# Kernel optimization log

Hardware: AMD Instinct MI355X
Metric: run time of the kernel (lower is better)

## Reference

```python
import jax, jax.numpy as jnp
import numpy as np

B, S, H, E, V = 16, 512, 1024, 256, 50257


def setup_inputs() -> dict:
    key = jax.random.key(0)
    ks = jax.random.split(key, 16)
    sc = 0.02
    return {
        "x": jax.random.randint(ks[0], (B, 1), 0, V),
        "dec_hs": jax.random.normal(ks[1], (1, B, H), jnp.float32),
        "enc_output": jax.random.normal(ks[2], (S, B, H), jnp.float32),
        "emb": jax.random.normal(ks[3], (V, E), jnp.float32) * sc,
        "w1_W": jax.random.normal(ks[4], (H, H), jnp.float32) * sc,
        "w1_b": jnp.zeros((H,), jnp.float32),
        "w2_W": jax.random.normal(ks[5], (H, H), jnp.float32) * sc,
        "w2_b": jnp.zeros((H,), jnp.float32),
        "va_W": jax.random.normal(ks[6], (1, H), jnp.float32) * sc,
        "va_b": jnp.zeros((1,), jnp.float32),
        "W_ih": jax.random.normal(ks[7], (3 * H, E + H), jnp.float32) * sc,
        "W_hh": jax.random.normal(ks[8], (3 * H, H), jnp.float32) * sc,
        "b_ih": jnp.zeros((3 * H,), jnp.float32),
        "b_hh": jnp.zeros((3 * H,), jnp.float32),
        "out_W": jax.random.normal(ks[9], (V, H), jnp.float32) * sc,
        "out_b": jnp.zeros((V,), jnp.float32),
    }


def reference(x, dec_hs, enc_output, emb, w1_W, w1_b, w2_W, w2_b, va_W, va_b,
              W_ih, W_hh, b_ih, b_hh, out_W, out_b):
    # --- Bahdanau attention ---
    # dec_hs: [1,B,H], enc_output: [S,B,H]
    dec_proj = dec_hs @ w1_W.T + w1_b           # [1,B,H]
    enc_proj = enc_output @ w2_W.T + w2_b       # [S,B,H]
    score = jnp.tanh(dec_proj + enc_proj) @ va_W.T + va_b  # [S,B,1]
    score = jnp.transpose(score, (1, 0, 2))     # [B,S,1]
    attn = jax.nn.softmax(score, axis=1)        # [B,S,1]
    context = jnp.sum(attn * jnp.transpose(enc_output, (1, 0, 2)), axis=1)  # [B,H]

    # --- embedding + concat (context first, as in torch.cat([ctx, emb])) ---
    e = emb[x[:, 0]]                            # [B,E]
    gru_in = jnp.concatenate([context, e], axis=-1)  # [B,H+E]

    # --- GRU single step; NOTE: original calls self.GRU(inp) without dec_hs,
    # so the initial hidden state is zeros (faithful to the source). ---
    h0 = jnp.zeros((gru_in.shape[0], w1_W.shape[0]), gru_in.dtype)  # [B,H]
    gi = gru_in @ W_ih.T + b_ih                 # [B,3H]
    gh = h0 @ W_hh.T + b_hh                     # [B,3H]
    i_r, i_z, i_n = jnp.split(gi, 3, axis=-1)
    h_r, h_z, h_n = jnp.split(gh, 3, axis=-1)
    r = jax.nn.sigmoid(i_r + h_r)
    z = jax.nn.sigmoid(i_z + h_z)
    n = jnp.tanh(i_n + r * h_n)
    h = (1.0 - z) * n + z * h0                  # [B,H]

    fc_out = h @ out_W.T + out_b                # [B,V]
    new_dec_hs = h[None]                        # [1,B,H]
    return fc_out, new_dec_hs, attn
```

## Files before the change

### kernel.cpp

```cpp
#include <hip/hip_runtime.h>
#include <hip/hip_bf16.h>

typedef unsigned short u16;
typedef __attribute__((ext_vector_type(4))) float f32x4;
typedef __attribute__((ext_vector_type(8))) __bf16 bf16x8;
typedef __attribute__((ext_vector_type(8))) unsigned short ushort8;

#define Bb 16
#define Ss 512
#define Hh 1024
#define Ee 256
#define Vv 50257
#define Mm 8192

#define WS_ENC_BF   0
#define WS_W2_BF    16777216
#define WS_DPW      18874368
#define WS_SCORE    18939904
#define WS_GRUIN    18972672
#define WS_GI       19054592
#define WS_HA_HI    19251200
#define WS_HA_LO    19283968

__device__ __forceinline__ u16 f2bf(float f) {
  unsigned u = __float_as_uint(f);
  return (u16)((u + 0x7FFFu + ((u >> 16) & 1u)) >> 16);
}

__device__ __forceinline__ void gl2lds16(const void* g, void* l) {
  __builtin_amdgcn_global_load_lds((__attribute__((address_space(1))) void*)g,
                                   (__attribute__((address_space(3))) void*)l,
                                   16, 0, 0);
}

__global__ __launch_bounds__(256) void k_cvt2(const float* __restrict__ enc, u16* __restrict__ encb,
                                              const float* __restrict__ w2, u16* __restrict__ w2b) {
  int i = blockIdx.x * 256 + threadIdx.x;
  const float* src; u16* dst; int j;
  if (i < 1048576) { src = enc; dst = encb; j = i; }
  else             { src = w2;  dst = w2b;  j = i - 1048576; }
  const float4* s4 = (const float4*)src;
  float4 a = s4[j * 2], c = s4[j * 2 + 1];
  ushort8 o;
  o[0] = f2bf(a.x); o[1] = f2bf(a.y); o[2] = f2bf(a.z); o[3] = f2bf(a.w);
  o[4] = f2bf(c.x); o[5] = f2bf(c.y); o[6] = f2bf(c.z); o[7] = f2bf(c.w);
  *(ushort8*)(dst + j * 8) = o;
}

__global__ __launch_bounds__(256) void k_prep(const float* __restrict__ dec_hs, const float* __restrict__ w1_W,
                                              const float* __restrict__ w1_b, const float* __restrict__ w2_b,
                                              const float* __restrict__ va_b, const int* __restrict__ x,
                                              const float* __restrict__ emb, float* __restrict__ dpw,
                                              float* __restrict__ score, float* __restrict__ gru_in) {
  const int n = blockIdx.x, t = threadIdx.x;
  float acc[16];
#pragma unroll
  for (int b = 0; b < 16; ++b) acc[b] = 0.f;
#pragma unroll
  for (int i = 0; i < 4; ++i) {
    int k = t + i * 256;
    float w = w1_W[n * Hh + k];
#pragma unroll
    for (int b = 0; b < 16; ++b) acc[b] = fmaf(w, dec_hs[b * Hh + k], acc[b]);
  }
#pragma unroll
  for (int m = 1; m < 64; m <<= 1)
#pragma unroll
    for (int b = 0; b < 16; ++b) acc[b] += __shfl_xor(acc[b], m, 64);
  __shared__ float red[4][16];
  int wave = t >> 6, lane = t & 63;
  if (lane == 0)
#pragma unroll
    for (int b = 0; b < 16; ++b) red[wave][b] = acc[b];
  __syncthreads();
  if (t < 16)
    dpw[t * Hh + n] = red[0][t] + red[1][t] + red[2][t] + red[3][t] + w1_b[n] + w2_b[n];
  int fid = n * 256 + t;
  if (fid < 16384) { int b = fid >> 10, k = fid & 1023; gru_in[b * 1280 + k] = 0.f; }
  int sid = fid - 16384;
  if (sid >= 0 && sid < Mm) score[sid] = va_b[0];
  int eid = fid - 24576;
  if (eid >= 0 && eid < 4096) { int b = eid >> 8, j = eid & 255; gru_in[b * 1280 + 1024 + j] = emb[x[b] * Ee + j]; }
}

__global__ __launch_bounds__(256) void k_gemm_score(const u16* __restrict__ A, const u16* __restrict__ Bm,
                                                    const float* __restrict__ dpw, const float* __restrict__ vaW,
                                                    float* __restrict__ score) {
  __shared__ __align__(16) u16 Al[4096];
  __shared__ __align__(16) u16 Bl[4096];
  const int tid = threadIdx.x;
  const int wave = tid >> 6, lane = tid & 63;
  const int quad = lane >> 4, l16 = lane & 15;
  const int m0 = blockIdx.x * 128, n0 = blockIdx.y * 128;
  const int wm = (wave & 1) * 64, wn = (wave >> 1) * 64;

  f32x4 acc[4][4];
#pragma unroll
  for (int i = 0; i < 4; ++i)
#pragma unroll
    for (int j = 0; j < 4; ++j) acc[i][j] = (f32x4){0.f, 0.f, 0.f, 0.f};

  const u16* gA = A + (m0 + (tid >> 2)) * 1024 + (tid & 3) * 8;
  const u16* gB = Bm + (n0 + (tid >> 2)) * 1024 + (tid & 3) * 8;
  u16* lA0 = &Al[(wave * 64) * 8];
  u16* lA1 = &Al[(256 + wave * 64) * 8];
  u16* lB0 = &Bl[(wave * 64) * 8];
  u16* lB1 = &Bl[(256 + wave * 64) * 8];

  for (int kt = 0; kt < 1024; kt += 32) {
    __syncthreads();
    gl2lds16(gA + kt, lA0);
    gl2lds16(gA + 64 * 1024 + kt, lA1);
    gl2lds16(gB + kt, lB0);
    gl2lds16(gB + 64 * 1024 + kt, lB1);
    __syncthreads();
    bf16x8 af[4], bfr[4];
#pragma unroll
    for (int i = 0; i < 4; ++i) {
      af[i]  = *(const bf16x8*)&Al[(wm + i * 16 + l16) * 32 + quad * 8];
      bfr[i] = *(const bf16x8*)&Bl[(wn + i * 16 + l16) * 32 + quad * 8];
    }
#pragma unroll
    for (int i = 0; i < 4; ++i)
#pragma unroll
      for (int j = 0; j < 4; ++j)
        acc[i][j] = __builtin_amdgcn_mfma_f32_16x16x32_bf16(af[i], bfr[j], acc[i][j], 0, 0, 0);
  }

  __syncthreads();
  float* dpw_t = (float*)Al;
  float* va_t  = (float*)Bl;
  for (int idx = tid; idx < 2048; idx += 256) {
    int b = idx >> 7, nn = idx & 127;
    dpw_t[idx] = dpw[b * Hh + n0 + nn];
  }
  if (tid < 128) va_t[tid] = vaW[n0 + tid];
  __syncthreads();

  float rs[4][4];
#pragma unroll
  for (int i = 0; i < 4; ++i)
#pragma unroll
    for (int r = 0; r < 4; ++r) rs[i][r] = 0.f;
#pragma unroll
  for (int i = 0; i < 4; ++i)
#pragma unroll
    for (int j = 0; j < 4; ++j) {
      int nn = wn + j * 16 + l16;
      float va = va_t[nn];
#pragma unroll
      for (int r = 0; r < 4; ++r) {
        float xv = acc[i][j][r] + dpw_t[(quad * 4 + r) * 128 + nn];
        rs[i][r] += tanhf(xv) * va;
      }
    }
#pragma unroll
  for (int i = 0; i < 4; ++i)
#pragma unroll
    for (int r = 0; r < 4; ++r) {
      float v = rs[i][r];
      v += __shfl_xor(v, 1, 64);
      v += __shfl_xor(v, 2, 64);
      v += __shfl_xor(v, 4, 64);
      v += __shfl_xor(v, 8, 64);
      if (l16 == 0) atomicAdd(&score[m0 + wm + i * 16 + quad * 4 + r], v);
    }
}

__global__ __launch_bounds__(256) void k_softmax(const float* __restrict__ score, float* __restrict__ attn) {
  const int b = blockIdx.x, t = threadIdx.x;
  __shared__ float red[256];
  float v0 = score[t * Bb + b];
  float v1 = score[(t + 256) * Bb + b];
  red[t] = fmaxf(v0, v1);
  __syncthreads();
  for (int s = 128; s > 0; s >>= 1) { if (t < s) red[t] = fmaxf(red[t], red[t + s]); __syncthreads(); }
  float mx = red[0];
  __syncthreads();
  float e0 = expf(v0 - mx), e1 = expf(v1 - mx);
  red[t] = e0 + e1;
  __syncthreads();
  for (int s = 128; s > 0; s >>= 1) { if (t < s) red[t] += red[t + s]; __syncthreads(); }
  float inv = 1.f / red[0];
  attn[b * Ss + t] = e0 * inv;
  attn[b * Ss + t + 256] = e1 * inv;
}

__global__ __launch_bounds__(256) void k_context(const float* __restrict__ attn, const float* __restrict__ enc,
                                                 float* __restrict__ gru_in) {
  const int b = blockIdx.x, sc = blockIdx.y, t = threadIdx.x;
  const int s0 = sc * 16;
  float acc[4] = {0.f, 0.f, 0.f, 0.f};
  for (int s = s0; s < s0 + 16; ++s) {
    float a = attn[b * Ss + s];
    const float* e = enc + (s * Bb + b) * Hh;
#pragma unroll
    for (int hh = 0; hh < 4; ++hh) acc[hh] = fmaf(a, e[t + hh * 256], acc[hh]);
  }
#pragma unroll
  for (int hh = 0; hh < 4; ++hh) atomicAdd(&gru_in[b * 1280 + t + hh * 256], acc[hh]);
}

__global__ __launch_bounds__(256) void k_gi(const float* __restrict__ W_ih, const float* __restrict__ gru_in,
                                            const float* __restrict__ b_ih, float* __restrict__ gi) {
  const int n = blockIdx.x, t = threadIdx.x;
  float acc[16];
#pragma unroll
  for (int b = 0; b < 16; ++b) acc[b] = 0.f;
#pragma unroll
  for (int i = 0; i < 5; ++i) {
    int k = t + i * 256;
    float w = W_ih[n * 1280 + k];
#pragma unroll
    for (int b = 0; b < 16; ++b) acc[b] = fmaf(w, gru_in[b * 1280 + k], acc[b]);
  }
#pragma unroll
  for (int m = 1; m < 64; m <<= 1)
#pragma unroll
    for (int b = 0; b < 16; ++b) acc[b] += __shfl_xor(acc[b], m, 64);
  __shared__ float red[4][16];
  int wave = t >> 6, lane = t & 63;
  if (lane == 0)
#pragma unroll
    for (int b = 0; b < 16; ++b) red[wave][b] = acc[b];
  __syncthreads();
  if (t < 16)
    gi[t * 3072 + n] = red[0][t] + red[1][t] + red[2][t] + red[3][t] + b_ih[n];
}

__global__ __launch_bounds__(256) void k_gates(const float* __restrict__ gi, const float* __restrict__ b_hh,
                                               float* __restrict__ h_out, u16* __restrict__ hA_hi,
                                               u16* __restrict__ hA_lo) {
  int idx = blockIdx.x * 256 + threadIdx.x;
  int b = idx >> 10, j = idx & 1023;
  float ir = gi[b * 3072 + j], iz = gi[b * 3072 + 1024 + j], in_ = gi[b * 3072 + 2048 + j];
  float r = 1.f / (1.f + expf(-(ir + b_hh[j])));
  float z = 1.f / (1.f + expf(-(iz + b_hh[1024 + j])));
  float n = tanhf(in_ + r * b_hh[2048 + j]);
  float hv = (1.f - z) * n;
  h_out[idx] = hv;
  u16 hi = f2bf(hv);
  float hi_f = __uint_as_float((unsigned)hi << 16);
  u16 lo = f2bf(hv - hi_f);
  int g = j >> 3, jj = j & 7;
  hA_hi[g * 128 + b * 8 + jj] = hi;
  hA_lo[g * 128 + b * 8 + jj] = lo;
}

__global__ __launch_bounds__(256) void k_fc(const float* __restrict__ out_W, const float* __restrict__ out_b,
                                            const u16* __restrict__ hA_hi, const u16* __restrict__ hA_lo,
                                            float* __restrict__ fc) {
  __shared__ __align__(16) float tile[128 * 128];
  const int tid = threadIdx.x;
  const int wave = tid >> 6, lane = tid & 63;
  const int quad = lane >> 4, l16 = lane & 15;
  const int v0 = blockIdx.x * 128;

  f32x4 acc[2];
  acc[0] = (f32x4){0.f, 0.f, 0.f, 0.f};
  acc[1] = (f32x4){0.f, 0.f, 0.f, 0.f};

  for (int c = 0; c < 8; ++c) {
    __syncthreads();
#pragma unroll
    for (int i = 0; i < 16; ++i) {
      int r = wave * 32 + i * 2 + (lane >> 5);
      int gg = (lane & 31) ^ (r & 7);
      int vrow = v0 + r;
      if (vrow > Vv - 1) vrow = Vv - 1;
      const float* g = out_W + (long)vrow * Hh + c * 128 + gg * 4;
      float* l = tile + (wave * 32 + i * 2) * 128;
      gl2lds16(g, l);
    }
    __syncthreads();
#pragma unroll
    for (int s = 0; s < 4; ++s) {
      int gbase = c * 16 + s * 4 + quad;
      bf16x8 a_hi = *(const bf16x8*)(hA_hi + gbase * 128 + l16 * 8);
      bf16x8 a_lo = *(const bf16x8*)(hA_lo + gbase * 128 + l16 * 8);
#pragma unroll
      for (int t = 0; t < 2; ++t) {
        int vl = wave * 32 + t * 16 + l16;
        int m0 = s * 8 + quad * 2;
        int p0 = m0 ^ (vl & 7), p1 = (m0 + 1) ^ (vl & 7);
        const float* rowp = tile + vl * 128;
        f32x4 w0 = *(const f32x4*)(rowp + p0 * 4);
        f32x4 w1 = *(const f32x4*)(rowp + p1 * 4);
        union { ushort8 u; bf16x8 b; } bu;
        bu.u[0] = f2bf(w0[0]); bu.u[1] = f2bf(w0[1]); bu.u[2] = f2bf(w0[2]); bu.u[3] = f2bf(w0[3]);
        bu.u[4] = f2bf(w1[0]); bu.u[5] = f2bf(w1[1]); bu.u[6] = f2bf(w1[2]); bu.u[7] = f2bf(w1[3]);
        acc[t] = __builtin_amdgcn_mfma_f32_16x16x32_bf16(a_hi, bu.b, acc[t], 0, 0, 0);
        acc[t] = __builtin_amdgcn_mfma_f32_16x16x32_bf16(a_lo, bu.b, acc[t], 0, 0, 0);
      }
    }
  }

#pragma unroll
  for (int t = 0; t < 2; ++t) {
    int v = v0 + wave * 32 + t * 16 + l16;
    if (v < Vv) {
      float ob = out_b[v];
#pragma unroll
      for (int r = 0; r < 4; ++r)
        fc[(long)(quad * 4 + r) * Vv + v] = acc[t][r] + ob;
    }
  }
}

extern "C" void kernel_launch(void* const* d_in, const int* in_sizes, int n_in,
                              void* d_out, int out_size, void* d_ws, size_t ws_size,
                              hipStream_t stream) {
  const int*   x       = (const int*)d_in[0];
  const float* dec_hs  = (const float*)d_in[1];
  const float* enc_out = (const float*)d_in[2];
  const float* emb     = (const float*)d_in[3];
  const float* w1_W    = (const float*)d_in[4];
  const float* w1_b    = (const float*)d_in[5];
  const float* w2_W    = (const float*)d_in[6];
  const float* w2_b    = (const float*)d_in[7];
  const float* va_W    = (const float*)d_in[8];
  const float* va_b    = (const float*)d_in[9];
  const float* W_ih    = (const float*)d_in[10];
  const float* b_ih    = (const float*)d_in[12];
  const float* b_hh    = (const float*)d_in[13];
  const float* out_W   = (const float*)d_in[14];
  const float* out_b   = (const float*)d_in[15];

  char* ws = (char*)d_ws;
  u16*   enc_bf = (u16*)(ws + WS_ENC_BF);
  u16*   w2_bf  = (u16*)(ws + WS_W2_BF);
  float* dpw    = (float*)(ws + WS_DPW);
  float* score  = (float*)(ws + WS_SCORE);
  float* gru_in = (float*)(ws + WS_GRUIN);
  float* gi     = (float*)(ws + WS_GI);
  u16*   hA_hi  = (u16*)(ws + WS_HA_HI);
  u16*   hA_lo  = (u16*)(ws + WS_HA_LO);

  float* fc       = (float*)d_out;
  float* h_out    = fc + (long)Bb * Vv;
  float* attn_out = h_out + Bb * Hh;

  k_cvt2<<<4608, 256, 0, stream>>>(enc_out, enc_bf, w2_W, w2_bf);
  k_prep<<<1024, 256, 0, stream>>>(dec_hs, w1_W, w1_b, w2_b, va_b, x, emb, dpw, score, gru_in);
  k_gemm_score<<<dim3(64, 8), 256, 0, stream>>>(enc_bf, w2_bf, dpw, va_W, score);
  k_softmax<<<16, 256, 0, stream>>>(score, attn_out);
  k_context<<<dim3(16, 32), 256, 0, stream>>>(attn_out, enc_out, gru_in);
  k_gi<<<3072, 256, 0, stream>>>(W_ih, gru_in, b_ih, gi);
  k_gates<<<64, 256, 0, stream>>>(gi, b_hh, h_out, hA_hi, hA_lo);
  k_fc<<<(Vv + 127) / 128, 256, 0, stream>>>(out_W, out_b, hA_hi, hA_lo, fc);
}
```

Measured before the change: 450.2 us.

## Stream out_W directly to registers in FC kernel, dropping LDS staging

The FC projection kernel no longer stages out_W tiles through shared memory with barriers. Each lane now loads its own 8-float slice of a weight row from global memory and converts it to bf16 for MFMA, with 64 vocabulary rows per block instead of 128. The hi and lo accumulations use separate accumulators, which breaks the serial dependency between back-to-back MFMAs. This removes LDS traffic and syncs in this memory-bound GEMV-like kernel, but each lane's 32-byte reads are strided across rows, which may hurt coalescing.

```diff
diff --git a/kernel.cpp b/kernel.cpp
--- a/kernel.cpp
+++ b/kernel.cpp
@@ -250,60 +250,36 @@
 __global__ __launch_bounds__(256) void k_fc(const float* __restrict__ out_W, const float* __restrict__ out_b,
                                             const u16* __restrict__ hA_hi, const u16* __restrict__ hA_lo,
                                             float* __restrict__ fc) {
-  __shared__ __align__(16) float tile[128 * 128];
   const int tid = threadIdx.x;
   const int wave = tid >> 6, lane = tid & 63;
   const int quad = lane >> 4, l16 = lane & 15;
-  const int v0 = blockIdx.x * 128;
-
-  f32x4 acc[2];
-  acc[0] = (f32x4){0.f, 0.f, 0.f, 0.f};
-  acc[1] = (f32x4){0.f, 0.f, 0.f, 0.f};
-
-  for (int c = 0; c < 8; ++c) {
-    __syncthreads();
-#pragma unroll
-    for (int i = 0; i < 16; ++i) {
-      int r = wave * 32 + i * 2 + (lane >> 5);
-      int gg = (lane & 31) ^ (r & 7);
-      int vrow = v0 + r;
-      if (vrow > Vv - 1) vrow = Vv - 1;
-      const float* g = out_W + (long)vrow * Hh + c * 128 + gg * 4;
-      float* l = tile + (wave * 32 + i * 2) * 128;
-      gl2lds16(g, l);
-    }
-    __syncthreads();
-#pragma unroll
-    for (int s = 0; s < 4; ++s) {
-      int gbase = c * 16 + s * 4 + quad;
-      bf16x8 a_hi = *(const bf16x8*)(hA_hi + gbase * 128 + l16 * 8);
-      bf16x8 a_lo = *(const bf16x8*)(hA_lo + gbase * 128 + l16 * 8);
-#pragma unroll
-      for (int t = 0; t < 2; ++t) {
-        int vl = wave * 32 + t * 16 + l16;
-        int m0 = s * 8 + quad * 2;
-        int p0 = m0 ^ (vl & 7), p1 = (m0 + 1) ^ (vl & 7);
-        const float* rowp = tile + vl * 128;
-        f32x4 w0 = *(const f32x4*)(rowp + p0 * 4);
-        f32x4 w1 = *(const f32x4*)(rowp + p1 * 4);
-        union { ushort8 u; bf16x8 b; } bu;
-        bu.u[0] = f2bf(w0[0]); bu.u[1] = f2bf(w0[1]); bu.u[2] = f2bf(w0[2]); bu.u[3] = f2bf(w0[3]);
-        bu.u[4] = f2bf(w1[0]); bu.u[5] = f2bf(w1[1]); bu.u[6] = f2bf(w1[2]); bu.u[7] = f2bf(w1[3]);
-        acc[t] = __builtin_amdgcn_mfma_f32_16x16x32_bf16(a_hi, bu.b, acc[t], 0, 0, 0);
-        acc[t] = __builtin_amdgcn_mfma_f32_16x16x32_bf16(a_lo, bu.b, acc[t], 0, 0, 0);
-      }
-    }
-  }
-
-#pragma unroll
-  for (int t = 0; t < 2; ++t) {
-    int v = v0 + wave * 32 + t * 16 + l16;
-    if (v < Vv) {
-      float ob = out_b[v];
-#pragma unroll
-      for (int r = 0; r < 4; ++r)
-        fc[(long)(quad * 4 + r) * Vv + v] = acc[t][r] + ob;
-    }
+  const int v = blockIdx.x * 64 + wave * 16 + l16;
+  const int vr = v < Vv ? v : (Vv - 1);
+  const float* wrow = out_W + (long)vr * Hh + quad * 8;
+  const u16* pa_hi = hA_hi + quad * 128 + l16 * 8;
+  const u16* pa_lo = hA_lo + quad * 128 + l16 * 8;
+
+  f32x4 acc0 = (f32x4){0.f, 0.f, 0.f, 0.f};
+  f32x4 acc1 = (f32x4){0.f, 0.f, 0.f, 0.f};
+
+#pragma unroll 4
+  for (int kw = 0; kw < 32; ++kw) {
+    bf16x8 a_hi = *(const bf16x8*)(pa_hi + kw * 512);
+    bf16x8 a_lo = *(const bf16x8*)(pa_lo + kw * 512);
+    f32x4 w0 = *(const f32x4*)(wrow + kw * 32);
+    f32x4 w1 = *(const f32x4*)(wrow + kw * 32 + 4);
+    union { ushort8 u; bf16x8 b; } bu;
+    bu.u[0] = f2bf(w0[0]); bu.u[1] = f2bf(w0[1]); bu.u[2] = f2bf(w0[2]); bu.u[3] = f2bf(w0[3]);
+    bu.u[4] = f2bf(w1[0]); bu.u[5] = f2bf(w1[1]); bu.u[6] = f2bf(w1[2]); bu.u[7] = f2bf(w1[3]);
+    acc0 = __builtin_amdgcn_mfma_f32_16x16x32_bf16(a_hi, bu.b, acc0, 0, 0, 0);
+    acc1 = __builtin_amdgcn_mfma_f32_16x16x32_bf16(a_lo, bu.b, acc1, 0, 0, 0);
+  }
+
+  if (v < Vv) {
+    float ob = out_b[v];
+#pragma unroll
+    for (int r = 0; r < 4; ++r)
+      fc[(long)(quad * 4 + r) * Vv + v] = acc0[r] + acc1[r] + ob;
   }
 }
 
@@ -347,5 +323,5 @@
   k_context<<<dim3(16, 32), 256, 0, stream>>>(attn_out, enc_out, gru_in);
   k_gi<<<3072, 256, 0, stream>>>(W_ih, gru_in, b_ih, gi);
   k_gates<<<64, 256, 0, stream>>>(gi, b_hh, h_out, hA_hi, hA_lo);
-  k_fc<<<(Vv + 127) / 128, 256, 0, stream>>>(out_W, out_b, hA_hi, hA_lo, fc);
-}
+  k_fc<<<(Vv + 63) / 64, 256, 0, stream>>>(out_W, out_b, hA_hi, hA_lo, fc);
+}
```

New measurement: 447.5 us. No clear change (-0.6%).
